# Kernel optimization log

Measured on AMD Instinct MI355X. Metric: run time of the kernel, lower is better.

The kernel has to match this reference:

```python
import jax, jax.numpy as jnp
import numpy as np

N, T, E, B = 50000, 16, 800000, 2000
EMB, ENC, DEC, OUT_LEN = 32, 64, 128, 25
NEG_SLOPE = 0.1
BN_EPS = 1e-5


def lrelu(x):
    return jnp.where(x >= 0, x, NEG_SLOPE * x)


def gru_encode(xs, Wih, Whh, bih, bhh):
    # xs: [T, N, in] -> final hidden [N, H]   (torch GRU gate order: r, z, n)
    H = Whh.shape[1]

    def step(h, x_t):
        gi = x_t @ Wih.T + bih
        gh = h @ Whh.T + bhh
        i_r, i_z, i_n = jnp.split(gi, 3, axis=-1)
        h_r, h_z, h_n = jnp.split(gh, 3, axis=-1)
        r = jax.nn.sigmoid(i_r + h_r)
        z = jax.nn.sigmoid(i_z + h_z)
        n = jnp.tanh(i_n + r * h_n)
        return (1.0 - z) * n + z * h, None

    h0 = jnp.zeros((xs.shape[1], H), xs.dtype)
    hT, _ = jax.lax.scan(step, h0, xs)
    return hT


def lstm_layer(xs, Wih, Whh, bih, bhh):
    # xs: [T, B, in] -> outputs [T, B, H]   (torch LSTM gate order: i, f, g, o)
    H = Whh.shape[1]

    def step(carry, x_t):
        h, c = carry
        g = x_t @ Wih.T + bih + h @ Whh.T + bhh
        i, f, gg, o = jnp.split(g, 4, axis=-1)
        c = jax.nn.sigmoid(f) * c + jax.nn.sigmoid(i) * jnp.tanh(gg)
        h = jax.nn.sigmoid(o) * jnp.tanh(c)
        return (h, c), h

    z0 = jnp.zeros((xs.shape[1], H), xs.dtype)
    _, hs = jax.lax.scan(step, (z0, z0), xs)
    return hs


def cgconv(x, src, dst, edge_attr, Wf, bf, Ws, bs, gamma, beta, mean, var):
    # PyG CGConv: z = [x_i, x_j, e]; msg = sigmoid(lin_f(z)) * softplus(lin_s(z));
    # out = x + BN(scatter_add(msg, i))
    z = jnp.concatenate([x[dst], x[src], edge_attr], axis=-1)  # [E, 2*ENC+2]
    msg = jax.nn.sigmoid(z @ Wf.T + bf) * jax.nn.softplus(z @ Ws.T + bs)
    agg = jax.ops.segment_sum(msg, dst, num_segments=N)  # [N, ENC]
    agg = (agg - mean) * jax.lax.rsqrt(var + BN_EPS) * gamma + beta
    return x + agg


def setup_inputs() -> dict:
    key = jax.random.key(0)
    ks = jax.random.split(key, 32)

    def rn(k, shape, scale=0.1):
        return jax.random.normal(k, shape, jnp.float32) * scale

    inp = {}
    inp["x"] = jax.random.normal(ks[0], (N, T, 2), jnp.float32)
    inp["edge_index"] = jax.random.randint(ks[1], (2, E), 0, N)
    inp["edge_attr"] = jax.random.normal(ks[2], (E, 2), jnp.float32)
    inp["target_index"] = jnp.sort(jax.random.randint(ks[3], (B,), 0, N))
    inp["W_ip"] = rn(ks[4], (EMB, 2)); inp["b_ip"] = jnp.zeros((EMB,), jnp.float32)
    inp["gru_Wih"] = rn(ks[5], (3 * ENC, EMB)); inp["gru_Whh"] = rn(ks[6], (3 * ENC, ENC))
    inp["gru_bih"] = jnp.zeros((3 * ENC,), jnp.float32); inp["gru_bhh"] = jnp.zeros((3 * ENC,), jnp.float32)
    inp["W_dyn"] = rn(ks[7], (ENC, ENC)); inp["b_dyn"] = jnp.zeros((ENC,), jnp.float32)
    Z = 2 * ENC + 2
    for i, base in ((1, 8), (2, 14)):
        inp[f"cg{i}_Wf"] = rn(ks[base], (ENC, Z)); inp[f"cg{i}_bf"] = jnp.zeros((ENC,), jnp.float32)
        inp[f"cg{i}_Ws"] = rn(ks[base + 1], (ENC, Z)); inp[f"cg{i}_bs"] = jnp.zeros((ENC,), jnp.float32)
        inp[f"cg{i}_gamma"] = jnp.ones((ENC,), jnp.float32); inp[f"cg{i}_beta"] = jnp.zeros((ENC,), jnp.float32)
        inp[f"cg{i}_mean"] = jnp.zeros((ENC,), jnp.float32); inp[f"cg{i}_var"] = jnp.ones((ENC,), jnp.float32)
    inp["W_nbrs"] = rn(ks[20], (ENC, ENC)); inp["b_nbrs"] = jnp.zeros((ENC,), jnp.float32)
    inp["lstm0_Wih"] = rn(ks[21], (4 * DEC, 2 * ENC)); inp["lstm0_Whh"] = rn(ks[22], (4 * DEC, DEC))
    inp["lstm0_bih"] = jnp.zeros((4 * DEC,), jnp.float32); inp["lstm0_bhh"] = jnp.zeros((4 * DEC,), jnp.float32)
    inp["lstm1_Wih"] = rn(ks[23], (4 * DEC, DEC)); inp["lstm1_Whh"] = rn(ks[24], (4 * DEC, DEC))
    inp["lstm1_bih"] = jnp.zeros((4 * DEC,), jnp.float32); inp["lstm1_bhh"] = jnp.zeros((4 * DEC,), jnp.float32)
    inp["W_op"] = rn(ks[25], (2, DEC)); inp["b_op"] = jnp.zeros((2,), jnp.float32)
    return inp


def reference(x, edge_index, edge_attr, target_index, W_ip, b_ip,
              gru_Wih, gru_Whh, gru_bih, gru_bhh, W_dyn, b_dyn,
              cg1_Wf, cg1_bf, cg1_Ws, cg1_bs, cg1_gamma, cg1_beta, cg1_mean, cg1_var,
              cg2_Wf, cg2_bf, cg2_Ws, cg2_bs, cg2_gamma, cg2_beta, cg2_mean, cg2_var,
              W_nbrs, b_nbrs,
              lstm0_Wih, lstm0_Whh, lstm0_bih, lstm0_bhh,
              lstm1_Wih, lstm1_Whh, lstm1_bih, lstm1_bhh, W_op, b_op):
    src, dst = edge_index[0], edge_index[1]
    # --- history encoder (GRU) ---
    h = lrelu(x @ W_ip.T + b_ip)                                  # [N, T, EMB]
    hT = gru_encode(h.transpose(1, 0, 2), gru_Wih, gru_Whh, gru_bih, gru_bhh)  # [N, ENC]
    hist = lrelu(lrelu(hT) @ W_dyn.T + b_dyn)                     # [N, ENC]
    # --- CGConv interaction x2 ---
    f = cgconv(hist, src, dst, edge_attr, cg1_Wf, cg1_bf, cg1_Ws, cg1_bs,
               cg1_gamma, cg1_beta, cg1_mean, cg1_var)
    f = cgconv(f, src, dst, edge_attr, cg2_Wf, cg2_bf, cg2_Ws, cg2_bs,
               cg2_gamma, cg2_beta, cg2_mean, cg2_var)
    tar = lrelu(f[target_index] @ W_nbrs.T + b_nbrs)              # [B, ENC]
    enc = jnp.concatenate([hist[target_index], tar], axis=-1)     # [B, 2*ENC]
    # --- LSTM decoder over repeated encoding ---
    xs = jnp.broadcast_to(enc, (OUT_LEN,) + enc.shape)            # [OUT_LEN, B, 2*ENC]
    hs = lstm_layer(xs, lstm0_Wih, lstm0_Whh, lstm0_bih, lstm0_bhh)
    hs = lstm_layer(hs, lstm1_Wih, lstm1_Whh, lstm1_bih, lstm1_bhh)
    fut = hs.transpose(1, 0, 2) @ W_op.T + b_op                   # [B, OUT_LEN, 2]
    return fut
```

## Files before the change

kernel.cpp:

```cpp
#include <hip/hip_runtime.h>
#include <math.h>

#define NN   50000
#define TT   16
#define EE   800000
#define BB   2000
#define EMBD 32
#define ENC  64
#define DEC  128
#define OUTL 25
#define BN_EPS 1e-5f

typedef short v8s __attribute__((ext_vector_type(8)));
typedef float v4f __attribute__((ext_vector_type(4)));
#define MFMA16(a,b,c) __builtin_amdgcn_mfma_f32_16x16x32_bf16((a),(b),(c),0,0,0)

__device__ __forceinline__ float lrelu(float v){ return v >= 0.f ? v : 0.1f*v; }
__device__ __forceinline__ float fsig(float v){ return __builtin_amdgcn_rcpf(1.f + __expf(-v)); }
__device__ __forceinline__ float ftanh(float v){ return 2.f*__builtin_amdgcn_rcpf(1.f + __expf(-2.f*v)) - 1.f; }
__device__ __forceinline__ float fsoftplus(float v){
    return v > 15.f ? v : __logf(1.f + __expf(v));
}
__device__ __forceinline__ float hsum(float4 a){ return (a.x+a.y)+(a.z+a.w); }

__device__ __forceinline__ unsigned short f2bf(float f){
    unsigned u = __float_as_uint(f);
    u = u + 0x7FFFu + ((u>>16)&1u);
    return (unsigned short)(u>>16);
}
__device__ __forceinline__ float bf2f(unsigned short s){ return __uint_as_float(((unsigned)s)<<16); }

__device__ __forceinline__ void tsplit(float v, unsigned short& hi, unsigned short& lo){
    unsigned u = __float_as_uint(v);
    hi = (unsigned short)(u >> 16);
    float r = v - __uint_as_float(u & 0xFFFF0000u);
    lo = (unsigned short)(__float_as_uint(r) >> 16);
}

__device__ __forceinline__ v8s as_v8s(int4 v){
    union { int4 i; v8s s; } u; u.i = v; return u.s;
}

__device__ __forceinline__ void cvt8(const float* p, v8s& hi, v8s& lo){
    float4 a0 = *(const float4*)p;
    float4 a1 = *(const float4*)(p+4);
    float av[8] = {a0.x,a0.y,a0.z,a0.w,a1.x,a1.y,a1.z,a1.w};
#pragma unroll
    for (int j=0;j<8;j++){
        unsigned short h = f2bf(av[j]);
        hi[j] = (short)h;
        lo[j] = (short)f2bf(av[j] - bf2f(h));
    }
}
__device__ __forceinline__ void lrelu_resplit(v8s hh, v8s hl, v8s& oh, v8s& ol){
#pragma unroll
    for (int j=0;j<8;j++){
        float v = bf2f((unsigned short)hh[j]) + bf2f((unsigned short)hl[j]);
        float a = lrelu(v);
        unsigned short h = f2bf(a);
        oh[j] = (short)h;
        ol[j] = (short)f2bf(a - bf2f(h));
    }
}

__device__ __forceinline__ void pf_item(const float* W, int K, int KB, int i,
                                        unsigned short* out){
    int l = i & 63, fb = i >> 6;
    int kb = fb % KB, nt = fb / KB;
    int n = nt*16 + (l&15);
    int k0 = kb*32 + ((l>>4)*8);
#pragma unroll
    for (int j=0;j<8;j++) out[i*8+j] = f2bf(W[(size_t)n*K + k0 + j]);
}
__device__ __forceinline__ void phl_item(const float* W, int K, int KB, int i,
                                         unsigned short* hi, unsigned short* lo){
    int l = i & 63, fb = i >> 6;
    int kb = fb % KB, nt = fb / KB;
    int n = nt*16 + (l&15);
    int k0 = kb*32 + ((l>>4)*8);
#pragma unroll
    for (int j=0;j<8;j++){
        float v = W[(size_t)n*K + k0 + j];
        unsigned short h = f2bf(v);
        hi[i*8+j] = h;
        lo[i*8+j] = f2bf(v - bf2f(h));
    }
}
__device__ __forceinline__ void pcat_item(const float* Wa, const float* Wb,
                                          int K1, int K, int KB, int i,
                                          unsigned short* out){
    int l = i & 63, fb = i >> 6;
    int kb = fb % KB, nt = fb / KB;
    int n = nt*16 + (l&15);
    int k0 = kb*32 + ((l>>4)*8);
#pragma unroll
    for (int j=0;j<8;j++){
        int k = k0 + j;
        float v = (k < K1) ? Wa[(size_t)n*K1 + k] : Wb[(size_t)n*(K-K1) + (k-K1)];
        out[i*8+j] = f2bf(v);
    }
}
__device__ __forceinline__ void pproj_item(const float* Wf, const float* Ws, int i,
                                           unsigned short* hi, unsigned short* lo){
    int l = i & 63, fb = i >> 6;
    int kb = fb & 1, nt = fb >> 1;
    int n = nt*16 + (l&15);
    int d = n >> 6, c = n & 63;
    const float* W = (d < 2) ? Wf : Ws;
    int k0 = (d&1)*64 + kb*32 + ((l>>4)*8);
#pragma unroll
    for (int j=0;j<8;j++){
        float v = W[c*130 + k0 + j];
        unsigned short h = f2bf(v);
        hi[i*8+j] = h;
        lo[i*8+j] = f2bf(v - bf2f(h));
    }
}

__global__ void pack_all(
    const float* __restrict__ gWih, const float* __restrict__ gWhh,
    const float* __restrict__ Wdyn,
    const float* __restrict__ l0Whh, const float* __restrict__ l1Wih,
    const float* __restrict__ l1Whh, const float* __restrict__ l0Wih,
    const float* __restrict__ c1Wf, const float* __restrict__ c1Ws,
    const float* __restrict__ c2Wf, const float* __restrict__ c2Ws,
    unsigned short* __restrict__ pWih, unsigned short* __restrict__ pWhh,
    unsigned short* __restrict__ pWdyn,
    unsigned short* __restrict__ B0h, unsigned short* __restrict__ B1h,
    unsigned short* __restrict__ P1h, unsigned short* __restrict__ P1l,
    unsigned short* __restrict__ P2h, unsigned short* __restrict__ P2l,
    unsigned short* __restrict__ GIh, unsigned short* __restrict__ GIl,
    int* __restrict__ cnt, int* __restrict__ gtot)
{
    int i = blockIdx.x*256 + threadIdx.x;
    if (i < 768){ pf_item(gWih, 32, 1, i, pWih); return; }   i -= 768;
    if (i < 1536){ pf_item(gWhh, 64, 2, i, pWhh); return; }  i -= 1536;
    if (i < 512){ pf_item(Wdyn, 64, 2, i, pWdyn); return; }  i -= 512;
    if (i < 8192){ pcat_item(l0Whh, l0Whh, 128, 128, 4, i, B0h); return; } i -= 8192;
    if (i < 16384){ pcat_item(l1Wih, l1Whh, 128, 256, 8, i, B1h); return; } i -= 16384;
    if (i < 2048){ pproj_item(c1Wf, c1Ws, i, P1h, P1l); return; } i -= 2048;
    if (i < 2048){ pproj_item(c2Wf, c2Ws, i, P2h, P2l); return; } i -= 2048;
    if (i < 8192){ phl_item(l0Wih, 128, 4, i, GIh, GIl); return; } i -= 8192;
    if (i < NN){ cnt[i] = 0; return; } i -= NN;
    if (i < 1){ gtot[0] = 0; return; }
}
#define PACK_TOTAL (768+1536+512+8192+16384+2048+2048+8192+NN+1)

__global__ __launch_bounds__(128) void encoder_mfma(
    const float* __restrict__ x,
    const float* __restrict__ Wip, const float* __restrict__ bip,
    const unsigned short* __restrict__ pWih,
    const unsigned short* __restrict__ pWhh,
    const float* __restrict__ bih, const float* __restrict__ bhh,
    const unsigned short* __restrict__ pWdyn,
    const float* __restrict__ bdyn,
    float* __restrict__ hist)
{
    __shared__ float sxt[512];
    __shared__ unsigned short hfh[2][1024], hfl[2][1024];
    const int tid = threadIdx.x;
    const int l   = tid & 63;
    const int w   = tid >> 6;
    const int ln  = l & 15, q = l >> 4;
    const int blk = blockIdx.x;

    for (int idx = tid; idx < 512; idx += 128){
        int m = idx >> 5, r = idx & 31;
        sxt[(r>>1)*32 + m*2 + (r&1)] = x[(size_t)blk*512 + idx];
    }
    for (int i = tid; i < 1024; i += 128){
        hfh[0][i]=0; hfl[0][i]=0; hfh[1][i]=0; hfl[1][i]=0;
    }

    float w0[8], w1[8], bk[8];
#pragma unroll
    for (int j = 0; j < 8; j++){
        int k = q*8 + j;
        w0[j] = Wip[2*k]; w1[j] = Wip[2*k+1]; bk[j] = bip[k];
    }

    float bR[2], bZ[2], bNI[2], bNH[2];
    float hprev[2][4];
#pragma unroll
    for (int u = 0; u < 2; u++){
        int g = 2*w + u;
        int c = g*16 + ln;
        bR[u]  = bih[c]       + bhh[c];
        bZ[u]  = bih[64 + c]  + bhh[64 + c];
        bNI[u] = bih[128 + c];
        bNH[u] = bhh[128 + c];
        hprev[u][0]=0.f; hprev[u][1]=0.f; hprev[u][2]=0.f; hprev[u][3]=0.f;
    }
    const v8s* FIH = (const v8s*)pWih;
    const v8s* FHH = (const v8s*)pWhh;
    const v8s* FDY = (const v8s*)pWdyn;
    __syncthreads();

    int p = 0;
#pragma unroll 1
    for (int t = 0; t < TT; t++){
        float2 xv = *(const float2*)&sxt[t*32 + ln*2];
        v8s eh, el;
#pragma unroll
        for (int j = 0; j < 8; j++){
            float e = lrelu(w0[j]*xv.x + w1[j]*xv.y + bk[j]);
            unsigned short h_, l_;
            tsplit(e, h_, l_);
            eh[j] = (short)h_; el[j] = (short)l_;
        }
        v8s h0h = *(const v8s*)&hfh[p][l*8];
        v8s h0l = *(const v8s*)&hfl[p][l*8];
        v8s h1h = *(const v8s*)&hfh[p][512 + l*8];
        v8s h1l = *(const v8s*)&hfl[p][512 + l*8];
#pragma unroll
        for (int u = 0; u < 2; u++){
            int g = 2*w + u;
            v4f aR = {bR[u],bR[u],bR[u],bR[u]};
            v4f aZ = {bZ[u],bZ[u],bZ[u],bZ[u]};
            v4f aNI= {bNI[u],bNI[u],bNI[u],bNI[u]};
            v4f aNH= {bNH[u],bNH[u],bNH[u],bNH[u]};
            v8s b;
            b = FIH[(g   )*64 + l];    aR = MFMA16(eh,b,aR);  aR = MFMA16(el,b,aR);
            b = FHH[(g*2+0)*64+l];     aR = MFMA16(h0h,b,aR); aR = MFMA16(h0l,b,aR);
            b = FHH[(g*2+1)*64+l];     aR = MFMA16(h1h,b,aR); aR = MFMA16(h1l,b,aR);
            b = FIH[(4+g )*64 + l];    aZ = MFMA16(eh,b,aZ);  aZ = MFMA16(el,b,aZ);
            b = FHH[((4+g)*2+0)*64+l]; aZ = MFMA16(h0h,b,aZ); aZ = MFMA16(h0l,b,aZ);
            b = FHH[((4+g)*2+1)*64+l]; aZ = MFMA16(h1h,b,aZ); aZ = MFMA16(h1l,b,aZ);
            b = FIH[(8+g )*64 + l];    aNI= MFMA16(eh,b,aNI); aNI= MFMA16(el,b,aNI);
            b = FHH[((8+g)*2+0)*64+l]; aNH= MFMA16(h0h,b,aNH);aNH= MFMA16(h0l,b,aNH);
            b = FHH[((8+g)*2+1)*64+l]; aNH= MFMA16(h1h,b,aNH);aNH= MFMA16(h1l,b,aNH);
#pragma unroll
            for (int i = 0; i < 4; i++){
                float r_ = fsig(aR[i]);
                float z_ = fsig(aZ[i]);
                float nn_ = ftanh(aNI[i] + r_*aNH[i]);
                float hn = (1.f - z_)*nn_ + z_*hprev[u][i];
                hprev[u][i] = hn;
                int row = q*4 + i, col = g*16 + ln;
                int off = (col>>5)*512 + (16*((col&31)>>3) + row)*8 + (col&7);
                unsigned short hh_, hl_;
                tsplit(hn, hh_, hl_);
                hfh[1-p][off] = hh_;
                hfl[1-p][off] = hl_;
            }
        }
        __syncthreads();
        p ^= 1;
    }
    {
        v8s a0h,a0l,a1h,a1l;
        lrelu_resplit(*(const v8s*)&hfh[p][l*8],       *(const v8s*)&hfl[p][l*8],       a0h, a0l);
        lrelu_resplit(*(const v8s*)&hfh[p][512 + l*8], *(const v8s*)&hfl[p][512 + l*8], a1h, a1l);
#pragma unroll
        for (int u = 0; u < 2; u++){
            int nt = 2*w + u;
            float bb = bdyn[nt*16 + ln];
            v4f acc = {bb,bb,bb,bb};
            v8s b;
            b = FDY[(nt*2+0)*64 + l]; acc = MFMA16(a0h,b,acc); acc = MFMA16(a0l,b,acc);
            b = FDY[(nt*2+1)*64 + l]; acc = MFMA16(a1h,b,acc); acc = MFMA16(a1l,b,acc);
#pragma unroll
            for (int i = 0; i < 4; i++){
                hist[(size_t)(blk*16 + q*4 + i)*64 + nt*16 + ln] = lrelu(acc[i]);
            }
        }
    }
}

__global__ __launch_bounds__(256) void proj_mfma(
    const float* __restrict__ xin,
    const unsigned short* __restrict__ Bh, const unsigned short* __restrict__ Bl,
    float* __restrict__ Af, float* __restrict__ Bf,
    float* __restrict__ As, float* __restrict__ Bs)
{
    __shared__ float sx[64*68];
    const int tid = threadIdx.x;
    const int l = tid & 63;
    const int w = tid >> 6;
    const int ln = l & 15, q = l >> 4;
    const int n0 = blockIdx.x*64;

    for (int i=tid;i<64*16;i+=256){
        int nn = i>>4, f4 = i&15;
        float4 v = {0.f,0.f,0.f,0.f};
        if (n0+nn < NN) v = ((const float4*)(xin + (size_t)(n0+nn)*64))[f4];
        *(float4*)&sx[nn*68 + f4*4] = v;
    }
    __syncthreads();

    v8s ah0,al0,ah1,al1;
    cvt8(&sx[(w*16+ln)*68 +      q*8], ah0, al0);
    cvt8(&sx[(w*16+ln)*68 + 32 + q*8], ah1, al1);

    const v8s* FH = (const v8s*)Bh;
    const v8s* FL = (const v8s*)Bl;
#pragma unroll 1
    for (int nt=0; nt<16; nt++){
        v8s bh0 = FH[(nt*2+0)*64 + l], bl0 = FL[(nt*2+0)*64 + l];
        v8s bh1 = FH[(nt*2+1)*64 + l], bl1 = FL[(nt*2+1)*64 + l];
        v4f acc = {0.f,0.f,0.f,0.f};
        acc = MFMA16(ah0,bh0,acc); acc = MFMA16(al0,bh0,acc); acc = MFMA16(ah0,bl0,acc);
        acc = MFMA16(ah1,bh1,acc); acc = MFMA16(al1,bh1,acc); acc = MFMA16(ah1,bl1,acc);
        int d = nt >> 2, col = (nt&3)*16 + ln;
        float* op = (d==0) ? Af : (d==1) ? Bf : (d==2) ? As : Bs;
#pragma unroll
        for (int i=0;i<4;i++){
            int node = n0 + w*16 + q*4 + i;
            if (node < NN) op[(size_t)node*64 + col] = acc[i];
        }
    }
}

__global__ void count_kernel(const int* __restrict__ ei, int* __restrict__ cnt){
    int e = blockIdx.x*256 + threadIdx.x;
    if (e < EE) atomicAdd(&cnt[ei[EE+e]], 1);
}

__global__ void alloc_kernel(const int* __restrict__ cnt, int* __restrict__ gtot,
                             int* __restrict__ off, int* __restrict__ cur){
    int n = blockIdx.x*256 + threadIdx.x;
    if (n >= NN) return;
    int c = cnt[n];
    int s = atomicAdd(gtot, c);
    off[n] = s;
    cur[n] = s;
}

__global__ void scatter_kernel(const int* __restrict__ ei, const float* __restrict__ ea,
                               int* __restrict__ cur, int4* __restrict__ recS){
    int e = blockIdx.x*256 + threadIdx.x;
    if (e >= EE) return;
    int d = ei[EE+e];
    int p = atomicAdd(&cur[d], 1);
    int4 r;
    r.x = ei[e];
    r.y = __float_as_int(ea[2*(size_t)e]);
    r.z = __float_as_int(ea[2*(size_t)e+1]);
    r.w = 0;
    recS[p] = r;
}

__global__ __launch_bounds__(256) void cg_agg(
    const float* __restrict__ xin,
    const int4* __restrict__ recS,
    const int* __restrict__ off, const int* __restrict__ cnt,
    const float* __restrict__ Wf, const float* __restrict__ bf,
    const float* __restrict__ Ws, const float* __restrict__ bs,
    const float* __restrict__ Af, const float* __restrict__ Bf,
    const float* __restrict__ As, const float* __restrict__ Bs,
    const float* __restrict__ gamma, const float* __restrict__ beta,
    const float* __restrict__ mean, const float* __restrict__ var,
    float* __restrict__ outp)
{
    const int tid = threadIdx.x;
    const int c = tid & 63, wid = tid >> 6;
    const int n = blockIdx.x*4 + wid;
    if (n >= NN) return;

    const float wf0 = Wf[c*130+128], wf1 = Wf[c*130+129], bfc = bf[c];
    const float ws0 = Ws[c*130+128], ws1 = Ws[c*130+129], bsc = bs[c];
    const float afd = Af[(size_t)n*64+c] + bfc, asd = As[(size_t)n*64+c] + bsc;
    const float* Bfc = Bf + c;
    const float* Bsc = Bs + c;

    float acc = 0.f;
    int i = off[n];
    const int i1 = i + cnt[n];
#pragma unroll 1
    for (; i+1 < i1; i += 2){
        int4 r0 = recS[i], r1 = recS[i+1];
        float e00 = __int_as_float(r0.y), e01 = __int_as_float(r0.z);
        float e10 = __int_as_float(r1.y), e11 = __int_as_float(r1.z);
        float bf0v = Bfc[(size_t)r0.x*64], bs0v = Bsc[(size_t)r0.x*64];
        float bf1v = Bfc[(size_t)r1.x*64], bs1v = Bsc[(size_t)r1.x*64];
        float gf0 = afd + bf0v + wf0*e00 + wf1*e01;
        float gs0 = asd + bs0v + ws0*e00 + ws1*e01;
        float gf1 = afd + bf1v + wf0*e10 + wf1*e11;
        float gs1 = asd + bs1v + ws0*e10 + ws1*e11;
        acc += fsig(gf0)*fsoftplus(gs0);
        acc += fsig(gf1)*fsoftplus(gs1);
    }
    if (i < i1){
        int4 r0 = recS[i];
        float e00 = __int_as_float(r0.y), e01 = __int_as_float(r0.z);
        float gf = afd + Bfc[(size_t)r0.x*64] + wf0*e00 + wf1*e01;
        float gs = asd + Bsc[(size_t)r0.x*64] + ws0*e00 + ws1*e01;
        acc += fsig(gf)*fsoftplus(gs);
    }
    float bn = (acc - mean[c])*rsqrtf(var[c]+BN_EPS)*gamma[c] + beta[c];
    outp[(size_t)n*64+c] = xin[(size_t)n*64+c] + bn;
}

__global__ __launch_bounds__(256) void target_kernel(
    const float* __restrict__ hist, const float* __restrict__ f2,
    const int* __restrict__ tgt,
    const float* __restrict__ Wn, const float* __restrict__ bn_,
    float* __restrict__ enc)
{
    const int tid=threadIdx.x;
    const int c = tid&63, q = tid>>6;
    const int b = blockIdx.x*4 + q;
    if (b>=BB) return;
    const int n = tgt[b];
    float a = bn_[c];
#pragma unroll
    for (int k=0;k<ENC;k++) a += Wn[c*64+k]*f2[(size_t)n*64+k];
    enc[(size_t)b*128 + 64 + c] = lrelu(a);
    enc[(size_t)b*128 + c]      = hist[(size_t)n*64+c];
}

__global__ __launch_bounds__(512) void gi0_mfma(
    const float* __restrict__ enc,
    const unsigned short* __restrict__ GIh, const unsigned short* __restrict__ GIl,
    const float* __restrict__ bih0, const float* __restrict__ bhh0,
    float* __restrict__ gi0)
{
    __shared__ float senc[16*132];
    const int tid = threadIdx.x;
    const int l = tid & 63;
    const int w = tid >> 6;
    const int ln = l & 15, q = l >> 4;
    const int b0 = blockIdx.x*16;

    for (int i=tid;i<16*32;i+=512){
        int row = i>>5, f4 = i&31;
        *(float4*)&senc[row*132 + f4*4] = ((const float4*)(enc + (size_t)(b0+row)*128))[f4];
    }
    __syncthreads();

    v8s ah[4], al[4];
#pragma unroll
    for (int kb=0;kb<4;kb++) cvt8(&senc[ln*132 + kb*32 + q*8], ah[kb], al[kb]);

    const v8s* FH = (const v8s*)GIh;
    const v8s* FL = (const v8s*)GIl;
#pragma unroll
    for (int u=0;u<4;u++){
        int nt = w*4 + u;
        int col = nt*16 + ln;
        float bb = bih0[col] + bhh0[col];
        v4f acc = {bb,bb,bb,bb};
#pragma unroll
        for (int kb=0;kb<4;kb++){
            v8s bh = FH[(nt*4+kb)*64 + l];
            v8s bl = FL[(nt*4+kb)*64 + l];
            acc = MFMA16(ah[kb],bh,acc); acc = MFMA16(al[kb],bh,acc); acc = MFMA16(ah[kb],bl,acc);
        }
#pragma unroll
        for (int i=0;i<4;i++)
            gi0[(size_t)(b0 + q*4 + i)*512 + col] = acc[i];
    }
}

#define LMB 16
__global__ __launch_bounds__(512)
__attribute__((amdgpu_waves_per_eu(2,2)))
void lstm_mfma(
    const float* __restrict__ gi0,
    const unsigned short* __restrict__ B0h,
    const unsigned short* __restrict__ B1h,
    const float* __restrict__ bih1, const float* __restrict__ bhh1,
    const float* __restrict__ Wop, const float* __restrict__ bop,
    float* __restrict__ outp)
{
    __shared__ int4 sW0[32*4*64];
    __shared__ unsigned short h0hi[2][4*512], h0lo[2][4*512];
    __shared__ unsigned short h1hi[2][4*512], h1lo[2][4*512];
    const int tid = threadIdx.x;
    const int l = tid & 63;
    const int w = tid >> 6;
    const int c = l & 15;
    const int q = l >> 4;
    const int j = w*16 + c;
    const int b0 = blockIdx.x*LMB;

    {
        const int4* F0 = (const int4*)B0h;
        for (int i=tid;i<32*4*64;i+=512) sW0[i] = F0[i];
    }
    for (int i=tid;i<4*512;i+=512){
        h0hi[0][i]=0; h0lo[0][i]=0; h0hi[1][i]=0; h0lo[1][i]=0;
        h1hi[0][i]=0; h1lo[0][i]=0; h1hi[1][i]=0; h1lo[1][i]=0;
    }

    int4 W1r[32];
    {
        const int4* F1 = (const int4*)B1h;
#pragma unroll
        for (int g=0;g<4;g++)
#pragma unroll
            for (int kb=0;kb<8;kb++) W1r[g*8+kb] = F1[((g*8+w)*8 + kb)*64 + l];
#pragma unroll
        for (int i=0;i<32;i++)
            asm volatile("" : "+v"(W1r[i].x), "+v"(W1r[i].y), "+v"(W1r[i].z), "+v"(W1r[i].w));
    }

    float rgi[4][4];
#pragma unroll
    for (int g=0;g<4;g++)
#pragma unroll
        for (int i=0;i<4;i++)
            rgi[g][i] = gi0[(size_t)(b0 + q*4 + i)*512 + g*128 + j];

    float b1[4];
#pragma unroll
    for (int g=0;g<4;g++) b1[g] = bih1[g*128+j] + bhh1[g*128+j];
    float c0[4] = {0,0,0,0}, c1[4] = {0,0,0,0};
    const float wop0 = Wop[j], wop1 = Wop[128 + j];
    const float bo0 = bop[0], bo1 = bop[1];
    const int kbw = j>>5, qw = (j>>3)&3, jw = j&7;
    __syncthreads();

    int p = 0;
#pragma unroll 1
    for (int t=0;t<OUTL;t++){
        v4f aH[4], aL[4];
#pragma unroll
        for (int g=0;g<4;g++){
            v4f t4 = {rgi[g][0], rgi[g][1], rgi[g][2], rgi[g][3]};
            aH[g] = t4;
            v4f z = {0.f,0.f,0.f,0.f};
            aL[g] = z;
        }
#pragma unroll
        for (int kb=0;kb<4;kb++){
            v8s ah = *(const v8s*)&h0hi[p][kb*512 + l*8];
            v8s al = *(const v8s*)&h0lo[p][kb*512 + l*8];
#pragma unroll
            for (int g=0;g<4;g++){
                v8s bfr = as_v8s(sW0[((g*8+w)*4 + kb)*64 + l]);
                aH[g] = MFMA16(ah, bfr, aH[g]);
                aL[g] = MFMA16(al, bfr, aL[g]);
            }
        }
#pragma unroll
        for (int i=0;i<4;i++){
            float gi_ = aH[0][i]+aL[0][i], gf_ = aH[1][i]+aL[1][i];
            float gg_ = aH[2][i]+aL[2][i], go_ = aH[3][i]+aL[3][i];
            c0[i] = fsig(gf_)*c0[i] + fsig(gi_)*ftanh(gg_);
            float hn = fsig(go_)*ftanh(c0[i]);
            int off = kbw*512 + (qw*16 + q*4 + i)*8 + jw;
            unsigned short h = f2bf(hn);
            h0hi[1-p][off] = h;
            h0lo[1-p][off] = f2bf(hn - bf2f(h));
        }
        __syncthreads();

        v4f bH[4], bL[4];
#pragma unroll
        for (int g=0;g<4;g++){
            v4f t4={b1[g],b1[g],b1[g],b1[g]}; bH[g]=t4;
            v4f z={0.f,0.f,0.f,0.f}; bL[g]=z;
        }
#pragma unroll
        for (int kb=0;kb<8;kb++){
            const unsigned short* hb = (kb<4) ? h0hi[1-p] : h1hi[p];
            const unsigned short* lb = (kb<4) ? h0lo[1-p] : h1lo[p];
            int kk = kb & 3;
            v8s ah = *(const v8s*)&hb[kk*512 + l*8];
            v8s al = *(const v8s*)&lb[kk*512 + l*8];
#pragma unroll
            for (int g=0;g<4;g++){
                bH[g] = MFMA16(ah, as_v8s(W1r[g*8+kb]), bH[g]);
                bL[g] = MFMA16(al, as_v8s(W1r[g*8+kb]), bL[g]);
            }
        }
        float h1new[4];
#pragma unroll
        for (int i=0;i<4;i++){
            float gi_ = bH[0][i]+bL[0][i], gf_ = bH[1][i]+bL[1][i];
            float gg_ = bH[2][i]+bL[2][i], go_ = bH[3][i]+bL[3][i];
            c1[i] = fsig(gf_)*c1[i] + fsig(gi_)*ftanh(gg_);
            h1new[i] = fsig(go_)*ftanh(c1[i]);
            int off = kbw*512 + (qw*16 + q*4 + i)*8 + jw;
            unsigned short h = f2bf(h1new[i]);
            h1hi[1-p][off] = h;
            h1lo[1-p][off] = f2bf(h1new[i] - bf2f(h));
        }

        {
            float v0[4], v1[4];
#pragma unroll
            for (int i=0;i<4;i++){ v0[i] = h1new[i]*wop0; v1[i] = h1new[i]*wop1; }
#pragma unroll
            for (int m=1;m<16;m<<=1){
#pragma unroll
                for (int i=0;i<4;i++){
                    v0[i] += __shfl_xor(v0[i], m);
                    v1[i] += __shfl_xor(v1[i], m);
                }
            }
            if (c == 0){
                if (w == 0){
#pragma unroll
                    for (int i=0;i<4;i++){ v0[i] += bo0; v1[i] += bo1; }
                }
#pragma unroll
                for (int i=0;i<4;i++){
                    size_t base = (size_t)(b0 + q*4 + i)*(OUTL*2) + t*2;
                    atomicAdd(&outp[base    ], v0[i]);
                    atomicAdd(&outp[base + 1], v1[i]);
                }
            }
        }
        p ^= 1;
    }
}

extern "C" void kernel_launch(void* const* d_in, const int* in_sizes, int n_in,
                              void* d_out, int out_size, void* d_ws, size_t ws_size,
                              hipStream_t stream)
{
    const float* x    = (const float*)d_in[0];
    const int*   ei   = (const int*)d_in[1];
    const float* ea   = (const float*)d_in[2];
    const int*   tgt  = (const int*)d_in[3];
    const float* Wip  = (const float*)d_in[4];
    const float* bip  = (const float*)d_in[5];
    const float* gWih = (const float*)d_in[6];
    const float* gWhh = (const float*)d_in[7];
    const float* gbih = (const float*)d_in[8];
    const float* gbhh = (const float*)d_in[9];
    const float* Wdyn = (const float*)d_in[10];
    const float* bdyn = (const float*)d_in[11];
    const float* c1Wf=(const float*)d_in[12]; const float* c1bf=(const float*)d_in[13];
    const float* c1Ws=(const float*)d_in[14]; const float* c1bs=(const float*)d_in[15];
    const float* c1g =(const float*)d_in[16]; const float* c1b =(const float*)d_in[17];
    const float* c1m =(const float*)d_in[18]; const float* c1v =(const float*)d_in[19];
    const float* c2Wf=(const float*)d_in[20]; const float* c2bf=(const float*)d_in[21];
    const float* c2Ws=(const float*)d_in[22]; const float* c2bs=(const float*)d_in[23];
    const float* c2g =(const float*)d_in[24]; const float* c2b =(const float*)d_in[25];
    const float* c2m =(const float*)d_in[26]; const float* c2v =(const float*)d_in[27];
    const float* Wn  =(const float*)d_in[28]; const float* bn_ =(const float*)d_in[29];
    const float* l0Wih=(const float*)d_in[30]; const float* l0Whh=(const float*)d_in[31];
    const float* l0bih=(const float*)d_in[32]; const float* l0bhh=(const float*)d_in[33];
    const float* l1Wih=(const float*)d_in[34]; const float* l1Whh=(const float*)d_in[35];
    const float* l1bih=(const float*)d_in[36]; const float* l1bhh=(const float*)d_in[37];
    const float* Wop =(const float*)d_in[38]; const float* bop=(const float*)d_in[39];

    float* ws = (float*)d_ws;
    size_t o = 0;
    float* hist = ws + o; o += (size_t)NN*ENC;
    float* f1   = ws + o; o += (size_t)NN*ENC;
    float* f2   = ws + o; o += (size_t)NN*ENC;
    float* Af   = ws + o; o += (size_t)NN*ENC;
    float* Bf   = ws + o; o += (size_t)NN*ENC;
    float* As   = ws + o; o += (size_t)NN*ENC;
    float* Bs   = ws + o; o += (size_t)NN*ENC;
    float* enc  = ws + o; o += (size_t)BB*2*ENC;
    float* gi0  = ws + o; o += (size_t)BB*4*DEC;
    unsigned short* pWih  = (unsigned short*)(ws + o); o += (size_t)12*64*8/2;
    unsigned short* pWhh  = (unsigned short*)(ws + o); o += (size_t)24*64*8/2;
    unsigned short* pWdyn = (unsigned short*)(ws + o); o += (size_t)8*64*8/2;
    unsigned short* B0h = (unsigned short*)(ws + o); o += (size_t)32*4*64*8/2;
    unsigned short* B1h = (unsigned short*)(ws + o); o += (size_t)32*8*64*8/2;
    unsigned short* P1h = (unsigned short*)(ws + o); o += (size_t)2048*8/2;
    unsigned short* P1l = (unsigned short*)(ws + o); o += (size_t)2048*8/2;
    unsigned short* P2h = (unsigned short*)(ws + o); o += (size_t)2048*8/2;
    unsigned short* P2l = (unsigned short*)(ws + o); o += (size_t)2048*8/2;
    unsigned short* GIh = (unsigned short*)(ws + o); o += (size_t)8192*8/2;
    unsigned short* GIl = (unsigned short*)(ws + o); o += (size_t)8192*8/2;
    int* cnt    = (int*)(ws + o); o += NN;
    int* offv   = (int*)(ws + o); o += NN+1;
    int* curv   = (int*)(ws + o); o += NN;
    int* gtot   = (int*)(ws + o); o += 1;
    o = (o + 3) & ~(size_t)3;
    int4* recS  = (int4*)(ws + o); o += (size_t)4*EE;

    pack_all<<<(PACK_TOTAL+255)/256, 256, 0, stream>>>(
        gWih, gWhh, Wdyn, l0Whh, l1Wih, l1Whh, l0Wih,
        c1Wf, c1Ws, c2Wf, c2Ws,
        pWih, pWhh, pWdyn, B0h, B1h, P1h, P1l, P2h, P2l, GIh, GIl, cnt, gtot);

    (void)hipMemsetAsync(d_out, 0, (size_t)out_size*sizeof(float), stream);

    count_kernel<<<(EE+255)/256, 256, 0, stream>>>(ei, cnt);
    alloc_kernel<<<(NN+255)/256, 256, 0, stream>>>(cnt, gtot, offv, curv);
    scatter_kernel<<<(EE+255)/256, 256, 0, stream>>>(ei, ea, curv, recS);

    encoder_mfma<<<NN/16, 128, 0, stream>>>(x, Wip, bip, pWih, pWhh, gbih, gbhh, pWdyn, bdyn, hist);

    proj_mfma<<<(NN+63)/64, 256, 0, stream>>>(hist, P1h, P1l, Af,Bf,As,Bs);
    cg_agg<<<(NN+3)/4, 256, 0, stream>>>(hist, recS, offv, cnt,
                                         c1Wf,c1bf,c1Ws,c1bs, Af,Bf,As,Bs,
                                         c1g,c1b,c1m,c1v, f1);

    proj_mfma<<<(NN+63)/64, 256, 0, stream>>>(f1, P2h, P2l, Af,Bf,As,Bs);
    cg_agg<<<(NN+3)/4, 256, 0, stream>>>(f1, recS, offv, cnt,
                                         c2Wf,c2bf,c2Ws,c2bs, Af,Bf,As,Bs,
                                         c2g,c2b,c2m,c2v, f2);

    target_kernel<<<(BB+3)/4, 256, 0, stream>>>(hist, f2, tgt, Wn, bn_, enc);

    gi0_mfma<<<BB/16, 512, 0, stream>>>(enc, GIh, GIl, l0bih, l0bhh, gi0);

    lstm_mfma<<<BB/LMB, 512, 0, stream>>>(gi0, B0h, B1h,
                                          l1bih, l1bhh, Wop, bop, (float*)d_out);
}
```

Measured before the change: 617.0 us.

## Split GRU encoder across four waves and XOR-swizzle hidden-state LDS layout

The encoder block grows from 2 to 4 waves, so each wave computes one 16-column gate tile instead of two. This shortens each wave's serial MFMA chain per timestep, at the cost of more barrier participants and duplicated input-embedding work. Hidden-state LDS reads and writes in both the encoder and the LSTM decoder now use an XOR swizzle on the row index to reduce bank conflicts. The GRU update is also rewritten as n + z*(h-n) to save one multiply.

Result: no change. 615.2 us (-0.3%).

```diff
diff --git a/kernel.cpp b/kernel.cpp
--- a/kernel.cpp
+++ b/kernel.cpp
@@ -146,7 +146,7 @@
 }
 #define PACK_TOTAL (768+1536+512+8192+16384+2048+2048+8192+NN+1)
 
-__global__ __launch_bounds__(128) void encoder_mfma(
+__global__ __launch_bounds__(256) void encoder_mfma(
     const float* __restrict__ x,
     const float* __restrict__ Wip, const float* __restrict__ bip,
     const unsigned short* __restrict__ pWih,
@@ -163,12 +163,13 @@
     const int w   = tid >> 6;
     const int ln  = l & 15, q = l >> 4;
     const int blk = blockIdx.x;
-
-    for (int idx = tid; idx < 512; idx += 128){
+    const int rsw = ((l>>1)&7)<<3;
+
+    for (int idx = tid; idx < 512; idx += 256){
         int m = idx >> 5, r = idx & 31;
         sxt[(r>>1)*32 + m*2 + (r&1)] = x[(size_t)blk*512 + idx];
     }
-    for (int i = tid; i < 1024; i += 128){
+    for (int i = tid; i < 1024; i += 256){
         hfh[0][i]=0; hfl[0][i]=0; hfh[1][i]=0; hfl[1][i]=0;
     }
 
@@ -179,21 +180,17 @@
         w0[j] = Wip[2*k]; w1[j] = Wip[2*k+1]; bk[j] = bip[k];
     }
 
-    float bR[2], bZ[2], bNI[2], bNH[2];
-    float hprev[2][4];
-#pragma unroll
-    for (int u = 0; u < 2; u++){
-        int g = 2*w + u;
-        int c = g*16 + ln;
-        bR[u]  = bih[c]       + bhh[c];
-        bZ[u]  = bih[64 + c]  + bhh[64 + c];
-        bNI[u] = bih[128 + c];
-        bNH[u] = bhh[128 + c];
-        hprev[u][0]=0.f; hprev[u][1]=0.f; hprev[u][2]=0.f; hprev[u][3]=0.f;
-    }
+    const int c = w*16 + ln;
+    const float bR  = bih[c]       + bhh[c];
+    const float bZ  = bih[64 + c]  + bhh[64 + c];
+    const float bNI = bih[128 + c];
+    const float bNH = bhh[128 + c];
+    float hprev[4] = {0.f,0.f,0.f,0.f};
+
     const v8s* FIH = (const v8s*)pWih;
     const v8s* FHH = (const v8s*)pWhh;
     const v8s* FDY = (const v8s*)pWdyn;
+    const int wbase = (c>>5)*512 + (16*((c&31)>>3))*8 + (c&7);
     __syncthreads();
 
     int p = 0;
@@ -208,61 +205,58 @@
             tsplit(e, h_, l_);
             eh[j] = (short)h_; el[j] = (short)l_;
         }
-        v8s h0h = *(const v8s*)&hfh[p][l*8];
-        v8s h0l = *(const v8s*)&hfl[p][l*8];
-        v8s h1h = *(const v8s*)&hfh[p][512 + l*8];
-        v8s h1l = *(const v8s*)&hfl[p][512 + l*8];
-#pragma unroll
-        for (int u = 0; u < 2; u++){
-            int g = 2*w + u;
-            v4f aR = {bR[u],bR[u],bR[u],bR[u]};
-            v4f aZ = {bZ[u],bZ[u],bZ[u],bZ[u]};
-            v4f aNI= {bNI[u],bNI[u],bNI[u],bNI[u]};
-            v4f aNH= {bNH[u],bNH[u],bNH[u],bNH[u]};
-            v8s b;
-            b = FIH[(g   )*64 + l];    aR = MFMA16(eh,b,aR);  aR = MFMA16(el,b,aR);
-            b = FHH[(g*2+0)*64+l];     aR = MFMA16(h0h,b,aR); aR = MFMA16(h0l,b,aR);
-            b = FHH[(g*2+1)*64+l];     aR = MFMA16(h1h,b,aR); aR = MFMA16(h1l,b,aR);
-            b = FIH[(4+g )*64 + l];    aZ = MFMA16(eh,b,aZ);  aZ = MFMA16(el,b,aZ);
-            b = FHH[((4+g)*2+0)*64+l]; aZ = MFMA16(h0h,b,aZ); aZ = MFMA16(h0l,b,aZ);
-            b = FHH[((4+g)*2+1)*64+l]; aZ = MFMA16(h1h,b,aZ); aZ = MFMA16(h1l,b,aZ);
-            b = FIH[(8+g )*64 + l];    aNI= MFMA16(eh,b,aNI); aNI= MFMA16(el,b,aNI);
-            b = FHH[((8+g)*2+0)*64+l]; aNH= MFMA16(h0h,b,aNH);aNH= MFMA16(h0l,b,aNH);
-            b = FHH[((8+g)*2+1)*64+l]; aNH= MFMA16(h1h,b,aNH);aNH= MFMA16(h1l,b,aNH);
-#pragma unroll
-            for (int i = 0; i < 4; i++){
-                float r_ = fsig(aR[i]);
-                float z_ = fsig(aZ[i]);
-                float nn_ = ftanh(aNI[i] + r_*aNH[i]);
-                float hn = (1.f - z_)*nn_ + z_*hprev[u][i];
-                hprev[u][i] = hn;
-                int row = q*4 + i, col = g*16 + ln;
-                int off = (col>>5)*512 + (16*((col&31)>>3) + row)*8 + (col&7);
-                unsigned short hh_, hl_;
-                tsplit(hn, hh_, hl_);
-                hfh[1-p][off] = hh_;
-                hfl[1-p][off] = hl_;
-            }
+        v8s h0h = *(const v8s*)&hfh[p][(l*8) ^ rsw];
+        v8s h0l = *(const v8s*)&hfl[p][(l*8) ^ rsw];
+        v8s h1h = *(const v8s*)&hfh[p][512 + ((l*8) ^ rsw)];
+        v8s h1l = *(const v8s*)&hfl[p][512 + ((l*8) ^ rsw)];
+
+        v4f aR = {bR,bR,bR,bR};
+        v4f aZ = {bZ,bZ,bZ,bZ};
+        v4f aNI= {bNI,bNI,bNI,bNI};
+        v4f aNH= {bNH,bNH,bNH,bNH};
+        v8s b;
+        b = FIH[(w   )*64 + l];    aR = MFMA16(eh,b,aR);  aR = MFMA16(el,b,aR);
+        b = FHH[(w*2+0)*64+l];     aR = MFMA16(h0h,b,aR); aR = MFMA16(h0l,b,aR);
+        b = FHH[(w*2+1)*64+l];     aR = MFMA16(h1h,b,aR); aR = MFMA16(h1l,b,aR);
+        b = FIH[(4+w )*64 + l];    aZ = MFMA16(eh,b,aZ);  aZ = MFMA16(el,b,aZ);
+        b = FHH[((4+w)*2+0)*64+l]; aZ = MFMA16(h0h,b,aZ); aZ = MFMA16(h0l,b,aZ);
+        b = FHH[((4+w)*2+1)*64+l]; aZ = MFMA16(h1h,b,aZ); aZ = MFMA16(h1l,b,aZ);
+        b = FIH[(8+w )*64 + l];    aNI= MFMA16(eh,b,aNI); aNI= MFMA16(el,b,aNI);
+        b = FHH[((8+w)*2+0)*64+l]; aNH= MFMA16(h0h,b,aNH);aNH= MFMA16(h0l,b,aNH);
+        b = FHH[((8+w)*2+1)*64+l]; aNH= MFMA16(h1h,b,aNH);aNH= MFMA16(h1l,b,aNH);
+
+#pragma unroll
+        for (int i = 0; i < 4; i++){
+            float r_ = fsig(aR[i]);
+            float z_ = fsig(aZ[i]);
+            float nn_ = ftanh(aNI[i] + r_*aNH[i]);
+            float hn = nn_ + z_*(hprev[i] - nn_);
+            hprev[i] = hn;
+            int row = q*4 + i;
+            int off = (wbase + row*8) ^ ((((row)>>1)&7)<<3);
+            unsigned short hh_, hl_;
+            tsplit(hn, hh_, hl_);
+            hfh[1-p][off] = hh_;
+            hfl[1-p][off] = hl_;
         }
         __syncthreads();
         p ^= 1;
     }
     {
         v8s a0h,a0l,a1h,a1l;
-        lrelu_resplit(*(const v8s*)&hfh[p][l*8],       *(const v8s*)&hfl[p][l*8],       a0h, a0l);
-        lrelu_resplit(*(const v8s*)&hfh[p][512 + l*8], *(const v8s*)&hfl[p][512 + l*8], a1h, a1l);
-#pragma unroll
-        for (int u = 0; u < 2; u++){
-            int nt = 2*w + u;
-            float bb = bdyn[nt*16 + ln];
-            v4f acc = {bb,bb,bb,bb};
-            v8s b;
-            b = FDY[(nt*2+0)*64 + l]; acc = MFMA16(a0h,b,acc); acc = MFMA16(a0l,b,acc);
-            b = FDY[(nt*2+1)*64 + l]; acc = MFMA16(a1h,b,acc); acc = MFMA16(a1l,b,acc);
-#pragma unroll
-            for (int i = 0; i < 4; i++){
-                hist[(size_t)(blk*16 + q*4 + i)*64 + nt*16 + ln] = lrelu(acc[i]);
-            }
+        lrelu_resplit(*(const v8s*)&hfh[p][(l*8) ^ rsw],
+                      *(const v8s*)&hfl[p][(l*8) ^ rsw],       a0h, a0l);
+        lrelu_resplit(*(const v8s*)&hfh[p][512 + ((l*8) ^ rsw)],
+                      *(const v8s*)&hfl[p][512 + ((l*8) ^ rsw)], a1h, a1l);
+        const int nt = w;
+        float bb = bdyn[nt*16 + ln];
+        v4f acc = {bb,bb,bb,bb};
+        v8s b;
+        b = FDY[(nt*2+0)*64 + l]; acc = MFMA16(a0h,b,acc); acc = MFMA16(a0l,b,acc);
+        b = FDY[(nt*2+1)*64 + l]; acc = MFMA16(a1h,b,acc); acc = MFMA16(a1l,b,acc);
+#pragma unroll
+        for (int i = 0; i < 4; i++){
+            hist[(size_t)(blk*16 + q*4 + i)*64 + nt*16 + ln] = lrelu(acc[i]);
         }
     }
 }
@@ -473,6 +467,7 @@
     const int q = l >> 4;
     const int j = w*16 + c;
     const int b0 = blockIdx.x*LMB;
+    const int lsw = ((l>>1)&7)<<3;
 
     {
         const int4* F0 = (const int4*)B0h;
@@ -524,8 +519,8 @@
         }
 #pragma unroll
         for (int kb=0;kb<4;kb++){
-            v8s ah = *(const v8s*)&h0hi[p][kb*512 + l*8];
-            v8s al = *(const v8s*)&h0lo[p][kb*512 + l*8];
+            v8s ah = *(const v8s*)&h0hi[p][kb*512 + ((l*8) ^ lsw)];
+            v8s al = *(const v8s*)&h0lo[p][kb*512 + ((l*8) ^ lsw)];
 #pragma unroll
             for (int g=0;g<4;g++){
                 v8s bfr = as_v8s(sW0[((g*8+w)*4 + kb)*64 + l]);
@@ -539,7 +534,8 @@
             float gg_ = aH[2][i]+aL[2][i], go_ = aH[3][i]+aL[3][i];
             c0[i] = fsig(gf_)*c0[i] + fsig(gi_)*ftanh(gg_);
             float hn = fsig(go_)*ftanh(c0[i]);
-            int off = kbw*512 + (qw*16 + q*4 + i)*8 + jw;
+            int row = q*4 + i;
+            int off = (kbw*512 + (qw*16 + row)*8 + jw) ^ (((row>>1)&7)<<3);
             unsigned short h = f2bf(hn);
             h0hi[1-p][off] = h;
             h0lo[1-p][off] = f2bf(hn - bf2f(h));
@@ -557,8 +553,8 @@
             const unsigned short* hb = (kb<4) ? h0hi[1-p] : h1hi[p];
             const unsigned short* lb = (kb<4) ? h0lo[1-p] : h1lo[p];
             int kk = kb & 3;
-            v8s ah = *(const v8s*)&hb[kk*512 + l*8];
-            v8s al = *(const v8s*)&lb[kk*512 + l*8];
+            v8s ah = *(const v8s*)&hb[kk*512 + ((l*8) ^ lsw)];
+            v8s al = *(const v8s*)&lb[kk*512 + ((l*8) ^ lsw)];
 #pragma unroll
             for (int g=0;g<4;g++){
                 bH[g] = MFMA16(ah, as_v8s(W1r[g*8+kb]), bH[g]);
@@ -572,7 +568,8 @@
             float gg_ = bH[2][i]+bL[2][i], go_ = bH[3][i]+bL[3][i];
             c1[i] = fsig(gf_)*c1[i] + fsig(gi_)*ftanh(gg_);
             h1new[i] = fsig(go_)*ftanh(c1[i]);
-            int off = kbw*512 + (qw*16 + q*4 + i)*8 + jw;
+            int row = q*4 + i;
+            int off = (kbw*512 + (qw*16 + row)*8 + jw) ^ (((row>>1)&7)<<3);
             unsigned short h = f2bf(h1new[i]);
             h1hi[1-p][off] = h;
             h1lo[1-p][off] = f2bf(h1new[i] - bf2f(h));
@@ -678,7 +675,7 @@
     alloc_kernel<<<(NN+255)/256, 256, 0, stream>>>(cnt, gtot, offv, curv);
     scatter_kernel<<<(EE+255)/256, 256, 0, stream>>>(ei, ea, curv, recS);
 
-    encoder_mfma<<<NN/16, 128, 0, stream>>>(x, Wip, bip, pWih, pWhh, gbih, gbhh, pWdyn, bdyn, hist);
+    encoder_mfma<<<NN/16, 256, 0, stream>>>(x, Wip, bip, pWih, pWhh, gbih, gbhh, pWdyn, bdyn, hist);
 
     proj_mfma<<<(NN+63)/64, 256, 0, stream>>>(hist, P1h, P1l, Af,Bf,As,Bs);
     cg_agg<<<(NN+3)/4, 256, 0, stream>>>(hist, recS, offv, cnt,
```
